# Kernel optimization log

Measured on AMD Instinct MI355X. Metric: run time of the kernel, lower is better.

The kernel has to match this reference:

```python
import jax, jax.numpy as jnp
from jax import lax
import numpy as np

N, E = 50000, 1600000
IN, HID, OUT, K = 512, 256, 40, 10
ALPHA = 0.1
BN_EPS = 1e-5


def setup_inputs() -> dict:
    key = jax.random.key(0)
    ks = jax.random.split(key, 8)
    x = jax.random.normal(ks[0], (N, IN), dtype=jnp.float32)
    edge_index = jax.random.randint(ks[1], (2, E), 0, N, dtype=jnp.int32)
    # lin1 / lin2 (torch Linear: y = x @ W.T + b)
    W1 = jax.random.normal(ks[2], (HID, IN), dtype=jnp.float32) / np.sqrt(IN)
    b1 = jnp.zeros((HID,), dtype=jnp.float32)
    W2 = jax.random.normal(ks[3], (OUT, HID), dtype=jnp.float32) / np.sqrt(HID)
    b2 = jnp.zeros((OUT,), dtype=jnp.float32)
    # BatchNorm1d params (eval mode: running stats)
    bn_weight = jnp.ones((HID,), dtype=jnp.float32)
    bn_bias = jnp.zeros((HID,), dtype=jnp.float32)
    bn_mean = jax.random.normal(ks[4], (HID,), dtype=jnp.float32) * 0.1
    bn_var = jax.random.uniform(ks[5], (HID,), dtype=jnp.float32, minval=0.5, maxval=1.5)
    # GPR polynomial coefficients gamma[k] = alpha*(1-alpha)^k, gamma[K]=(1-alpha)^K
    g = ALPHA * (1.0 - ALPHA) ** np.arange(K + 1, dtype=np.float32)
    g[-1] = (1.0 - ALPHA) ** K
    gamma = jnp.asarray(g)
    return {"x": x, "edge_index": edge_index, "W1": W1, "b1": b1,
            "bn_weight": bn_weight, "bn_bias": bn_bias, "bn_mean": bn_mean,
            "bn_var": bn_var, "W2": W2, "b2": b2, "gamma": gamma}


def reference(x, edge_index, W1, b1, bn_weight, bn_bias, bn_mean, bn_var, W2, b2, gamma):
    row, col = edge_index[0], edge_index[1]
    # symmetric-ish normalization: deg computed from row only (as in the torch code)
    deg = jax.ops.segment_sum(jnp.ones_like(row, dtype=x.dtype), row, num_segments=N)
    deg = jnp.clip(deg, 1.0, None)
    dinv = deg ** -0.5
    norm = dinv[row] * dinv[col]  # [E]
    # MLP: lin1 -> BN(eval) -> ReLU -> (dropout off in eval) -> lin2
    h = x @ W1.T + b1
    h = (h - bn_mean) * lax.rsqrt(bn_var + BN_EPS) * bn_weight + bn_bias
    h = jax.nn.relu(h)
    z = h @ W2.T + b2  # [N, OUT]

    def step(carry, g):
        h_k, acc = carry
        # h_new[col] += norm * h_k[row]  (SpMM via gather + segment_sum)
        h_new = jax.ops.segment_sum(norm[:, None] * h_k[row], col, num_segments=N)
        return (h_new, acc + g * h_new), None

    (_, hidden), _ = lax.scan(step, (z, gamma[0] * z), gamma[1:])
    return hidden
```

## Files before the change

### kernel.cpp

```cpp
#include <hip/hip_runtime.h>
#include <cstddef>

#define NN 50000
#define EE 1600000
#define IN_DIM 512
#define HID 256
#define OUT_DIM 40
#define KSTEPS 10
#define BN_EPS 1e-5f

#define HB 256
#define ECHUNK (EE / HB)
#define BNODE 40
#define NB 1280
#define HRW ((NN + 3) / 4)
#define SORTCAP 3072

typedef __attribute__((ext_vector_type(8))) short short8;
typedef __attribute__((ext_vector_type(4))) float f32x4;

__device__ inline unsigned short bf16_rne(float v) {
    union { float f; unsigned u; } c; c.f = v;
    unsigned u = c.u;
    unsigned r = u + 0x7fff + ((u >> 16) & 1);
    return (unsigned short)(r >> 16);
}
__device__ inline float bf16_to_f(unsigned short h) {
    union { unsigned u; float f; } c; c.u = ((unsigned)h) << 16;
    return c.f;
}
__device__ inline unsigned short f32_to_f16(float v) {
    union { _Float16 h; unsigned short u; } c; c.h = (_Float16)v; return c.u;
}
__device__ inline float f16_to_f32(unsigned short u) {
    union { unsigned short u; _Float16 h; } c; c.u = u; return (float)c.h;
}

__global__ __launch_bounds__(256) void k_hist(const int* __restrict__ ei,
                                              unsigned* __restrict__ histR8,
                                              int* __restrict__ histBT) {
    __shared__ unsigned hr[HRW];
    __shared__ int hb[NB];
    int b = blockIdx.x, tid = threadIdx.x;
    for (int i = tid; i < HRW; i += 256) hr[i] = 0;
    for (int i = tid; i < NB; i += 256) hb[i] = 0;
    __syncthreads();
    int e0 = b * ECHUNK;
    for (int e = e0 + tid; e < e0 + ECHUNK; e += 256) {
        int r = ei[e];
        int c = ei[EE + e];
        atomicAdd(&hr[r >> 2], 1u << ((r & 3) * 8));
        atomicAdd(&hb[(unsigned)c / BNODE], 1);
    }
    __syncthreads();
    unsigned* o = histR8 + (size_t)b * HRW;
    for (int i = tid; i < HRW; i += 256) o[i] = hr[i];
    for (int i = tid; i < NB; i += 256) histBT[(size_t)i * HB + b] = hb[i];
}

__global__ void k_dinv2(const unsigned* __restrict__ histR8, float* __restrict__ dinv) {
    int i = blockIdx.x * blockDim.x + threadIdx.x;
    if (i >= NN) return;
    int word = i >> 2, sh = (i & 3) * 8;
    int d = 0;
    for (int blk = 0; blk < HB; ++blk)
        d += (histR8[(size_t)blk * HRW + word] >> sh) & 0xFFu;
    float fd = d < 1 ? 1.0f : (float)d;
    dinv[i] = 1.0f / sqrtf(fd);
}

__global__ __launch_bounds__(256) void k_colsumB(int* __restrict__ histBT,
                                                 int* __restrict__ totB) {
    int wv = (blockIdx.x * 256 + threadIdx.x) >> 6;
    int lane = threadIdx.x & 63;
    if (wv >= NB) return;
    int4 v = ((int4*)(histBT + (size_t)wv * HB))[lane];
    int s = v.x + v.y + v.z + v.w;
    int p = s;
    for (int d = 1; d < 64; d <<= 1) {
        int t = __shfl_up(p, d);
        if (lane >= d) p += t;
    }
    int excl = p - s;
    int4 w;
    w.x = excl;
    w.y = excl + v.x;
    w.z = excl + v.x + v.y;
    w.w = excl + v.x + v.y + v.z;
    ((int4*)(histBT + (size_t)wv * HB))[lane] = w;
    if (lane == 63) totB[wv] = p;
}

__global__ __launch_bounds__(256) void k_scanT(const int* __restrict__ totB,
                                               int* __restrict__ bptr) {
    __shared__ int wsum[4];
    int tid = threadIdx.x;
    int loc[5], s = 0;
#pragma unroll
    for (int j = 0; j < 5; ++j) { loc[j] = totB[tid * 5 + j]; s += loc[j]; }
    int lane = tid & 63, w = tid >> 6, v = s;
    for (int d = 1; d < 64; d <<= 1) {
        int t = __shfl_up(v, d);
        if (lane >= d) v += t;
    }
    if (lane == 63) wsum[w] = v;
    __syncthreads();
    if (w == 0 && lane < 4) {
        int t = wsum[lane];
        for (int d = 1; d < 4; d <<= 1) {
            int u = __shfl_up(t, d);
            if (lane >= d) t += u;
        }
        wsum[lane] = t;
    }
    __syncthreads();
    int run = (w > 0 ? wsum[w - 1] : 0) + (v - s);
#pragma unroll
    for (int j = 0; j < 5; ++j) { bptr[tid * 5 + j] = run; run += loc[j]; }
    if (tid == 255) bptr[NB] = run;
}

__global__ __launch_bounds__(256) void k_scatterB(const int* __restrict__ ei,
                                                  const float* __restrict__ dinv,
                                                  const int* __restrict__ bptr,
                                                  const int* __restrict__ histBT,
                                                  int2* __restrict__ ep) {
    __shared__ int cur[NB];
    int b = blockIdx.x, tid = threadIdx.x;
    for (int i = tid; i < NB; i += 256) cur[i] = bptr[i] + histBT[(size_t)i * HB + b];
    __syncthreads();
    int e0 = b * ECHUNK;
    for (int e = e0 + tid; e < e0 + ECHUNK; e += 256) {
        int r = ei[e];
        int c = ei[EE + e];
        int bk = (unsigned)c / BNODE;
        int pos = atomicAdd(&cur[bk], 1);
        int2 p;
        p.x = r | ((c - bk * BNODE) << 16);
        p.y = __float_as_int(dinv[r] * dinv[c]);
        ep[pos] = p;
    }
}

__global__ __launch_bounds__(256) void k_sortB(const int* __restrict__ bptr,
                                               const int2* __restrict__ ep,
                                               unsigned* __restrict__ ep4,
                                               int* __restrict__ ptr) {
    __shared__ int2 buf[SORTCAP];
    __shared__ int h40[BNODE];
    __shared__ int pfx[BNODE + 1];
    int b = blockIdx.x, tid = threadIdx.x;
    int e0 = bptr[b], e1 = bptr[b + 1], n = e1 - e0;
    if (tid < BNODE) h40[tid] = 0;
    __syncthreads();
    for (int i = tid; i < n; i += 256) {
        int2 p = ep[e0 + i];
        buf[i] = p;
        atomicAdd(&h40[p.x >> 16], 1);
    }
    __syncthreads();
    if (tid == 0) {
        int run = 0;
#pragma unroll
        for (int j = 0; j < BNODE; ++j) { pfx[j] = run; run += h40[j]; }
        pfx[BNODE] = run;
    }
    __syncthreads();
    if (tid < BNODE) {
        int node = b * BNODE + tid;
        if (node < NN) ptr[node] = e0 + pfx[tid];
        h40[tid] = pfx[tid];
    }
    if (tid == 64 && b * BNODE + BNODE >= NN) ptr[NN] = e1;
    __syncthreads();
    for (int i = tid; i < n; i += 256) {
        int2 p = buf[i];
        int cl = p.x >> 16;
        int pos = atomicAdd(&h40[cl], 1);
        unsigned short hn = f32_to_f16(__int_as_float(p.y));
        ep4[e0 + pos] = (unsigned)(p.x & 0xFFFF) | ((unsigned)hn << 16);
    }
}

__global__ void k_w1split(const float* __restrict__ W1, unsigned short* __restrict__ w1h,
                          unsigned short* __restrict__ w1l) {
    int i = blockIdx.x * blockDim.x + threadIdx.x;
    if (i >= HID * IN_DIM) return;
    float v = W1[i];
    unsigned short h = bf16_rne(v);
    unsigned short l = bf16_rne(v - bf16_to_f(h));
    w1h[i] = h;
    w1l[i] = l;
}

#define BM 64
#define BK 32
__device__ inline int swzA(int row, int b) {
    return row * 64 + (b ^ (int)((((unsigned)row >> 1) & 3u) << 4));
}
__global__ __launch_bounds__(256, 6) void k_gemm1m(const float* __restrict__ x,
                                                   const unsigned short* __restrict__ w1h,
                                                   const unsigned short* __restrict__ w1l,
                                                   const float* __restrict__ b1,
                                                   const float* __restrict__ bnw,
                                                   const float* __restrict__ bnb,
                                                   const float* __restrict__ bnm,
                                                   const float* __restrict__ bnv,
                                                   float* __restrict__ h) {
    __shared__ __align__(16) unsigned short Ah[BM * BK];
    __shared__ __align__(16) unsigned short Al[BM * BK];
    __shared__ __align__(16) unsigned short Bh[128 * BK];
    __shared__ __align__(16) unsigned short Bl[128 * BK];
    int tid = threadIdx.x;
    int lane = tid & 63;
    int wn = tid >> 6;
    int brow = blockIdx.x * BM;
    int bcol = blockIdx.y * 128;

    int ra = tid >> 2, ck = tid & 3;
    int rb = tid >> 1, cbs = (tid & 1) * 16;

    bool rok = (brow + ra) < NN;
    const float* xa = x + (size_t)(brow + ra) * IN_DIM + ck * 8;
    const unsigned short* bhp = w1h + (size_t)(bcol + rb) * IN_DIM + cbs;
    const unsigned short* blp = w1l + (size_t)(bcol + rb) * IN_DIM + cbs;

    f32x4 acc[4][2];
#pragma unroll
    for (int i = 0; i < 4; ++i)
#pragma unroll
        for (int j = 0; j < 2; ++j) acc[i][j] = (f32x4){0.f, 0.f, 0.f, 0.f};

    int frA = lane & 15;
    int frB = wn * 32 + (lane & 15);
    int fko = (lane >> 4) * 16;

    for (int kt = 0; kt < IN_DIM; kt += BK) {
        float4 v0 = make_float4(0.f, 0.f, 0.f, 0.f), v1 = v0;
        if (rok) { v0 = *(const float4*)(xa + kt); v1 = *(const float4*)(xa + kt + 4); }
        short8 gh0 = *(const short8*)(bhp + kt);
        short8 gh1 = *(const short8*)(bhp + kt + 8);
        short8 gl0 = *(const short8*)(blp + kt);
        short8 gl1 = *(const short8*)(blp + kt + 8);
        union { unsigned short u[8]; short8 v; } uh, ul;
        {
            float vv[8] = {v0.x, v0.y, v0.z, v0.w, v1.x, v1.y, v1.z, v1.w};
#pragma unroll
            for (int j = 0; j < 8; ++j) {
                unsigned short hh = bf16_rne(vv[j]);
                uh.u[j] = hh;
                ul.u[j] = bf16_rne(vv[j] - bf16_to_f(hh));
            }
        }
        __syncthreads();
        {
            int ab = swzA(ra, ck * 16);
            *(short8*)((char*)Ah + ab) = uh.v;
            *(short8*)((char*)Al + ab) = ul.v;
            int bb0 = swzA(rb, cbs * 2);
            int bb1 = swzA(rb, cbs * 2 + 16);
            *(short8*)((char*)Bh + bb0) = gh0;
            *(short8*)((char*)Bh + bb1) = gh1;
            *(short8*)((char*)Bl + bb0) = gl0;
            *(short8*)((char*)Bl + bb1) = gl1;
        }
        __syncthreads();

        short8 afh[4], afl[4];
#pragma unroll
        for (int mi = 0; mi < 4; ++mi) {
            int byte = swzA(frA + mi * 16, fko);
            afh[mi] = *(short8*)((char*)Ah + byte);
            afl[mi] = *(short8*)((char*)Al + byte);
        }
#pragma unroll
        for (int ni = 0; ni < 2; ++ni) {
            int byte = swzA(frB + ni * 16, fko);
            short8 bh = *(short8*)((char*)Bh + byte);
            short8 bl = *(short8*)((char*)Bl + byte);
#pragma unroll
            for (int mi = 0; mi < 4; ++mi) {
                acc[mi][ni] = __builtin_amdgcn_mfma_f32_16x16x32_bf16(afh[mi], bh, acc[mi][ni], 0, 0, 0);
                acc[mi][ni] = __builtin_amdgcn_mfma_f32_16x16x32_bf16(afl[mi], bh, acc[mi][ni], 0, 0, 0);
                acc[mi][ni] = __builtin_amdgcn_mfma_f32_16x16x32_bf16(afh[mi], bl, acc[mi][ni], 0, 0, 0);
            }
        }
    }

    int cbase = bcol + wn * 32 + (lane & 15);
    float scl[2], off[2];
#pragma unroll
    for (int ni = 0; ni < 2; ++ni) {
        int c = cbase + ni * 16;
        float s = bnw[c] * rsqrtf(bnv[c] + BN_EPS);
        scl[ni] = s;
        off[ni] = (b1[c] - bnm[c]) * s + bnb[c];
    }
#pragma unroll
    for (int mi = 0; mi < 4; ++mi) {
        int r0 = brow + mi * 16 + ((lane >> 4) << 2);
#pragma unroll
        for (int ni = 0; ni < 2; ++ni) {
            int c = cbase + ni * 16;
#pragma unroll
            for (int j = 0; j < 4; ++j) {
                int r = r0 + j;
                if (r < NN) {
                    float v = acc[mi][ni][j] * scl[ni] + off[ni];
                    h[(size_t)r * HID + c] = v > 0.f ? v : 0.f;
                }
            }
        }
    }
}

__global__ __launch_bounds__(256) void k_gemm2(const float* __restrict__ h,
                                               const float* __restrict__ W2,
                                               const float* __restrict__ b2,
                                               const float* __restrict__ gamma,
                                               unsigned short* __restrict__ ping,
                                               float* __restrict__ out) {
    __shared__ float W2T[HID * OUT_DIM];
    int tid = threadIdx.x;
    for (int i = tid; i < HID * OUT_DIM; i += 256) {
        int o = i / HID;
        int k = i - o * HID;
        W2T[k * OUT_DIM + o] = W2[i];
    }
    __syncthreads();
    int n = blockIdx.x * 256 + tid;
    if (n >= NN) return;

    float4 acc[10];
#pragma unroll
    for (int o4 = 0; o4 < 10; ++o4) acc[o4] = *(const float4*)&b2[o4 * 4];

    const float4* hr = (const float4*)(h + (size_t)n * HID);
    const float4* wt = (const float4*)W2T;
    for (int j = 0; j < HID / 4; ++j) {
        float4 hv = hr[j];
#pragma unroll
        for (int c = 0; c < 4; ++c) {
            float hk = (c == 0) ? hv.x : (c == 1) ? hv.y : (c == 2) ? hv.z : hv.w;
            const float4* wr = wt + (size_t)(j * 4 + c) * 10;
#pragma unroll
            for (int o4 = 0; o4 < 10; ++o4) {
                float4 w = wr[o4];
                acc[o4].x += hk * w.x;
                acc[o4].y += hk * w.y;
                acc[o4].z += hk * w.z;
                acc[o4].w += hk * w.w;
            }
        }
    }
    float g0 = gamma[0];
    uint2* pp = (uint2*)(ping + (size_t)n * OUT_DIM);
    float4* op = (float4*)(out + (size_t)n * OUT_DIM);
#pragma unroll
    for (int o4 = 0; o4 < 10; ++o4) {
        uint2 w;
        w.x = (unsigned)bf16_rne(acc[o4].x) | ((unsigned)bf16_rne(acc[o4].y) << 16);
        w.y = (unsigned)bf16_rne(acc[o4].z) | ((unsigned)bf16_rne(acc[o4].w) << 16);
        pp[o4] = w;
        float4 g;
        g.x = g0 * acc[o4].x; g.y = g0 * acc[o4].y;
        g.z = g0 * acc[o4].z; g.w = g0 * acc[o4].w;
        op[o4] = g;
    }
}

__global__ __launch_bounds__(256) void k_spmm5(const int* __restrict__ ptr,
                                               const unsigned* __restrict__ ep4,
                                               const unsigned short* __restrict__ cur,
                                               unsigned short* __restrict__ nxt,
                                               float* __restrict__ out,
                                               const float* __restrict__ gamma, int k) {
    int wave = (blockIdx.x * blockDim.x + threadIdx.x) >> 6;
    int lane = threadIdx.x & 63;
    if (wave >= NN) return;
    int e0 = ptr[wave], e1 = ptr[wave + 1];
    int es = lane / 10;
    int fq = lane - es * 10;
    bool act = es < 6;
    float a0 = 0.f, a1 = 0.f, a2 = 0.f, a3 = 0.f;

    for (int base = e0; base < e1; base += 48) {
        unsigned q[8];
#pragma unroll
        for (int g = 0; g < 8; ++g) {
            int e = base + g * 6 + es;
            q[g] = (act && e < e1) ? ep4[e] : 0u;
        }
#pragma unroll
        for (int g = 0; g < 8; ++g) {
            int src = (int)(q[g] & 0xFFFFu);
            float nm = f16_to_f32((unsigned short)(q[g] >> 16));
            uint2 u = *((const uint2*)(cur + (size_t)src * OUT_DIM) + fq);
            a0 += nm * __uint_as_float(u.x << 16);
            a1 += nm * __uint_as_float(u.x & 0xFFFF0000u);
            a2 += nm * __uint_as_float(u.y << 16);
            a3 += nm * __uint_as_float(u.y & 0xFFFF0000u);
        }
    }
    float s0 = a0, s1 = a1, s2 = a2, s3 = a3;
#pragma unroll
    for (int j = 1; j < 6; ++j) {
        s0 += __shfl(a0, fq + j * 10);
        s1 += __shfl(a1, fq + j * 10);
        s2 += __shfl(a2, fq + j * 10);
        s3 += __shfl(a3, fq + j * 10);
    }
    if (lane < 10) {
        uint2 w;
        w.x = (unsigned)bf16_rne(s0) | ((unsigned)bf16_rne(s1) << 16);
        w.y = (unsigned)bf16_rne(s2) | ((unsigned)bf16_rne(s3) << 16);
        *((uint2*)(nxt + (size_t)wave * OUT_DIM) + lane) = w;
        float gk = gamma[k];
        float4* op = (float4*)(out + (size_t)wave * OUT_DIM) + lane;
        float4 ov = *op;
        ov.x += gk * s0; ov.y += gk * s1; ov.z += gk * s2; ov.w += gk * s3;
        *op = ov;
    }
}

extern "C" void kernel_launch(void* const* d_in, const int* in_sizes, int n_in,
                              void* d_out, int out_size, void* d_ws, size_t ws_size,
                              hipStream_t stream) {
    const float* x   = (const float*)d_in[0];
    const int*   ei  = (const int*)d_in[1];
    const float* W1  = (const float*)d_in[2];
    const float* b1  = (const float*)d_in[3];
    const float* bnw = (const float*)d_in[4];
    const float* bnb = (const float*)d_in[5];
    const float* bnm = (const float*)d_in[6];
    const float* bnv = (const float*)d_in[7];
    const float* W2  = (const float*)d_in[8];
    const float* b2  = (const float*)d_in[9];
    const float* gamma = (const float*)d_in[10];
    float* out = (float*)d_out;

    char* ws = (char*)d_ws;
    const size_t A = 256;
    auto pad = [&](size_t b) { return (b + A - 1) / A * A; };
    size_t off = 0;
    int*      bptr  = (int*)     (ws + off); off += pad((size_t)(NB + 1) * 4);
    int*      totB  = (int*)     (ws + off); off += pad((size_t)NB * 4);
    float*    dinv  = (float*)   (ws + off); off += pad((size_t)NN * 4);
    int*      ptr   = (int*)     (ws + off); off += pad((size_t)(NN + 1) * 4);
    int2*     ep    = (int2*)    (ws + off); off += pad((size_t)EE * 8);
    unsigned* ep4   = (unsigned*)(ws + off); off += pad((size_t)EE * 4);
    float*    h     = (float*)   (ws + off); off += pad((size_t)NN * HID * 4);
    unsigned short* ping = (unsigned short*)(ws + off); off += pad((size_t)NN * OUT_DIM * 2);
    unsigned short* pong = (unsigned short*)(ws + off); off += pad((size_t)NN * OUT_DIM * 2);
    unsigned short* w1h  = (unsigned short*)(ws + off); off += pad((size_t)HID * IN_DIM * 2);
    unsigned short* w1l  = (unsigned short*)(ws + off); off += pad((size_t)HID * IN_DIM * 2);

    unsigned* histR8 = (unsigned*)h;
    int* histBT = (int*)((char*)h + (size_t)HB * HRW * 4);

    k_hist<<<HB, 256, 0, stream>>>(ei, histR8, histBT);
    k_dinv2<<<(NN + 255) / 256, 256, 0, stream>>>(histR8, dinv);
    k_colsumB<<<(NB * 64 + 255) / 256, 256, 0, stream>>>(histBT, totB);
    k_scanT<<<1, 256, 0, stream>>>(totB, bptr);
    k_scatterB<<<HB, 256, 0, stream>>>(ei, dinv, bptr, histBT, ep);
    k_sortB<<<NB, 256, 0, stream>>>(bptr, ep, ep4, ptr);

    k_w1split<<<(HID * IN_DIM + 255) / 256, 256, 0, stream>>>(W1, w1h, w1l);
    dim3 g1((NN + BM - 1) / BM, 2);
    k_gemm1m<<<g1, 256, 0, stream>>>(x, w1h, w1l, b1, bnw, bnb, bnm, bnv, h);
    k_gemm2<<<(NN + 255) / 256, 256, 0, stream>>>(h, W2, b2, gamma, ping, out);

    unsigned short* cur = ping;
    unsigned short* nxt = pong;
    for (int k = 1; k <= KSTEPS; ++k) {
        k_spmm5<<<(NN * 64 + 255) / 256, 256, 0, stream>>>(ptr, ep4, cur, nxt, out, gamma, k);
        unsigned short* t = cur; cur = nxt; nxt = t;
    }
}
```

Baseline: 430.3 us.

## Defer GPR gamma accumulation to one final kernel over stored bf16 iterates

Previously every propagation step did a read-modify-write of the full fp32 output, and gemm2 also wrote gamma0*z. Now each SpMM step writes its bf16 iterate into its own slice of the dead hidden buffer, and a single k_final kernel reads all eleven iterates and writes out once. The aim is to remove ten rounds of fp32 output traffic from the step kernels. In exchange, the accumulated terms are the bf16-rounded iterates rather than the fp32 sums, which slightly reduces precision. It also relies on the h buffer being free after gemm2.

```diff
diff --git a/kernel.cpp b/kernel.cpp
--- a/kernel.cpp
+++ b/kernel.cpp
@@ -317,9 +317,7 @@
 __global__ __launch_bounds__(256) void k_gemm2(const float* __restrict__ h,
                                                const float* __restrict__ W2,
                                                const float* __restrict__ b2,
-                                               const float* __restrict__ gamma,
-                                               unsigned short* __restrict__ ping,
-                                               float* __restrict__ out) {
+                                               unsigned short* __restrict__ hbuf0) {
     __shared__ float W2T[HID * OUT_DIM];
     int tid = threadIdx.x;
     for (int i = tid; i < HID * OUT_DIM; i += 256) {
@@ -353,28 +351,20 @@
             }
         }
     }
-    float g0 = gamma[0];
-    uint2* pp = (uint2*)(ping + (size_t)n * OUT_DIM);
-    float4* op = (float4*)(out + (size_t)n * OUT_DIM);
+    uint2* pp = (uint2*)(hbuf0 + (size_t)n * OUT_DIM);
 #pragma unroll
     for (int o4 = 0; o4 < 10; ++o4) {
         uint2 w;
         w.x = (unsigned)bf16_rne(acc[o4].x) | ((unsigned)bf16_rne(acc[o4].y) << 16);
         w.y = (unsigned)bf16_rne(acc[o4].z) | ((unsigned)bf16_rne(acc[o4].w) << 16);
         pp[o4] = w;
-        float4 g;
-        g.x = g0 * acc[o4].x; g.y = g0 * acc[o4].y;
-        g.z = g0 * acc[o4].z; g.w = g0 * acc[o4].w;
-        op[o4] = g;
     }
 }
 
 __global__ __launch_bounds__(256) void k_spmm5(const int* __restrict__ ptr,
                                                const unsigned* __restrict__ ep4,
                                                const unsigned short* __restrict__ cur,
-                                               unsigned short* __restrict__ nxt,
-                                               float* __restrict__ out,
-                                               const float* __restrict__ gamma, int k) {
+                                               unsigned short* __restrict__ nxt) {
     int wave = (blockIdx.x * blockDim.x + threadIdx.x) >> 6;
     int lane = threadIdx.x & 63;
     if (wave >= NN) return;
@@ -415,12 +405,33 @@
         w.x = (unsigned)bf16_rne(s0) | ((unsigned)bf16_rne(s1) << 16);
         w.y = (unsigned)bf16_rne(s2) | ((unsigned)bf16_rne(s3) << 16);
         *((uint2*)(nxt + (size_t)wave * OUT_DIM) + lane) = w;
-        float gk = gamma[k];
-        float4* op = (float4*)(out + (size_t)wave * OUT_DIM) + lane;
-        float4 ov = *op;
-        ov.x += gk * s0; ov.y += gk * s1; ov.z += gk * s2; ov.w += gk * s3;
-        *op = ov;
-    }
+    }
+}
+
+__global__ __launch_bounds__(256) void k_final(const unsigned short* __restrict__ hbuf0,
+                                               const unsigned short* __restrict__ hchain,
+                                               const float* __restrict__ gamma,
+                                               float* __restrict__ out) {
+    int idx = blockIdx.x * 256 + threadIdx.x;
+    if (idx >= NN * 10) return;
+    float g[KSTEPS + 1];
+#pragma unroll
+    for (int k = 0; k <= KSTEPS; ++k) g[k] = gamma[k];
+
+    uint2 v = *((const uint2*)hbuf0 + idx);
+    float a0 = g[0] * __uint_as_float(v.x << 16);
+    float a1 = g[0] * __uint_as_float(v.x & 0xFFFF0000u);
+    float a2 = g[0] * __uint_as_float(v.y << 16);
+    float a3 = g[0] * __uint_as_float(v.y & 0xFFFF0000u);
+#pragma unroll
+    for (int k = 1; k <= KSTEPS; ++k) {
+        uint2 u = *((const uint2*)(hchain + (size_t)(k - 1) * NN * OUT_DIM) + idx);
+        a0 += g[k] * __uint_as_float(u.x << 16);
+        a1 += g[k] * __uint_as_float(u.x & 0xFFFF0000u);
+        a2 += g[k] * __uint_as_float(u.y << 16);
+        a3 += g[k] * __uint_as_float(u.y & 0xFFFF0000u);
+    }
+    ((float4*)out)[idx] = make_float4(a0, a1, a2, a3);
 }
 
 extern "C" void kernel_launch(void* const* d_in, const int* in_sizes, int n_in,
@@ -450,13 +461,13 @@
     int2*     ep    = (int2*)    (ws + off); off += pad((size_t)EE * 8);
     unsigned* ep4   = (unsigned*)(ws + off); off += pad((size_t)EE * 4);
     float*    h     = (float*)   (ws + off); off += pad((size_t)NN * HID * 4);
-    unsigned short* ping = (unsigned short*)(ws + off); off += pad((size_t)NN * OUT_DIM * 2);
-    unsigned short* pong = (unsigned short*)(ws + off); off += pad((size_t)NN * OUT_DIM * 2);
-    unsigned short* w1h  = (unsigned short*)(ws + off); off += pad((size_t)HID * IN_DIM * 2);
-    unsigned short* w1l  = (unsigned short*)(ws + off); off += pad((size_t)HID * IN_DIM * 2);
+    unsigned short* hbuf0 = (unsigned short*)(ws + off); off += pad((size_t)NN * OUT_DIM * 2);
+    unsigned short* w1h   = (unsigned short*)(ws + off); off += pad((size_t)HID * IN_DIM * 2);
+    unsigned short* w1l   = (unsigned short*)(ws + off); off += pad((size_t)HID * IN_DIM * 2);
 
     unsigned* histR8 = (unsigned*)h;
     int* histBT = (int*)((char*)h + (size_t)HB * HRW * 4);
+    unsigned short* hchain = (unsigned short*)h;
 
     k_hist<<<HB, 256, 0, stream>>>(ei, histR8, histBT);
     k_dinv2<<<(NN + 255) / 256, 256, 0, stream>>>(histR8, dinv);
@@ -468,12 +479,14 @@
     k_w1split<<<(HID * IN_DIM + 255) / 256, 256, 0, stream>>>(W1, w1h, w1l);
     dim3 g1((NN + BM - 1) / BM, 2);
     k_gemm1m<<<g1, 256, 0, stream>>>(x, w1h, w1l, b1, bnw, bnb, bnm, bnv, h);
-    k_gemm2<<<(NN + 255) / 256, 256, 0, stream>>>(h, W2, b2, gamma, ping, out);
-
-    unsigned short* cur = ping;
-    unsigned short* nxt = pong;
+    k_gemm2<<<(NN + 255) / 256, 256, 0, stream>>>(h, W2, b2, hbuf0);
+
     for (int k = 1; k <= KSTEPS; ++k) {
-        k_spmm5<<<(NN * 64 + 255) / 256, 256, 0, stream>>>(ptr, ep4, cur, nxt, out, gamma, k);
-        unsigned short* t = cur; cur = nxt; nxt = t;
-    }
-}
+        const unsigned short* cur = (k == 1) ? hbuf0
+                                             : hchain + (size_t)(k - 2) * NN * OUT_DIM;
+        unsigned short* nxt = hchain + (size_t)(k - 1) * NN * OUT_DIM;
+        k_spmm5<<<(NN * 64 + 255) / 256, 256, 0, stream>>>(ptr, ep4, cur, nxt);
+    }
+
+    k_final<<<(NN * 10 + 255) / 256, 256, 0, stream>>>(hbuf0, hchain, gamma, out);
+}
```

Result: faster. 406.6 us (-5.5%).
